# Optimization experiments

Hardware: AMD Instinct MI355X
Metric: run time of the kernel (lower is better)

Reference implementation:

```python
import jax, jax.numpy as jnp
import numpy as np

B, S, D = 2, 2048, 1024
H, DH = 16, 64          # n_heads, d_head = d_model // n_heads
WINDOW = 128            # sliding-window size (causal, includes self)


def setup_inputs() -> dict:
    key = jax.random.key(0)
    k1, k2, k3 = jax.random.split(key, 3)
    x = jax.random.normal(k1, (B, S, D), dtype=jnp.float32)
    w_qkv = jax.random.normal(k2, (D, 3 * D), dtype=jnp.float32) * (1.0 / np.sqrt(D))
    w_out = jax.random.normal(k3, (D, D), dtype=jnp.float32) * (1.0 / np.sqrt(D))
    return {"x": x, "w_qkv": w_qkv, "w_out": w_out}


def reference(x, w_qkv, w_out):
    b, s, d = x.shape
    # QKV projection (no bias): [B,S,3D] -> [B,S,3,H,DH]
    qkv = (x @ w_qkv).reshape(b, s, 3, H, DH)
    q, k, v = qkv[:, :, 0], qkv[:, :, 1], qkv[:, :, 2]  # each [B,S,H,DH]
    scale = 1.0 / np.sqrt(DH)
    # Dense scores [B,H,S,S], as the explicit-mask SDPA path computes
    scores = jnp.einsum("bihd,bjhd->bhij", q, k) * scale
    i = jnp.arange(s)[:, None]
    j = jnp.arange(s)[None, :]
    # allowed: causal AND within sliding window of WINDOW positions (incl. self)
    allowed = (j <= i) & (j > i - WINDOW)
    scores = jnp.where(allowed, scores, -jnp.inf)
    attn = jax.nn.softmax(scores, axis=-1)
    out = jnp.einsum("bhij,bjhd->bihd", attn, v).reshape(b, s, d)
    return out @ w_out
```

## Files before the change

kernel.cpp:

```cpp
#include <hip/hip_runtime.h>

#define SQ      2048
#define NB      2
#define NH      16
#define DHD     64
#define WIN     128
#define DMODEL  1024
#define TRIPLE  3072

typedef __attribute__((ext_vector_type(8))) short  short8;
typedef __attribute__((ext_vector_type(4))) float  f32x4;

__device__ __forceinline__ unsigned short f2bf(float f) {
  unsigned u = __float_as_uint(f);
  u += 0x7fff + ((u >> 16) & 1);
  return (unsigned short)(u >> 16);
}

__device__ __forceinline__ void load_lds16(const void* g, void* l) {
  __builtin_amdgcn_global_load_lds(
      (const __attribute__((address_space(1))) unsigned int*)g,
      (__attribute__((address_space(3))) unsigned int*)l, 16, 0, 0);
}

__global__ __launch_bounds__(256) void prep_kernel(
    const float* __restrict__ x, const float* __restrict__ w_qkv,
    const float* __restrict__ w_out,
    unsigned short* __restrict__ xb, unsigned short* __restrict__ wqkvT,
    unsigned short* __restrict__ woutT) {
  __shared__ float tile[32][33];
  int blk = blockIdx.x, tid = threadIdx.x;
  if (blk < 4096) {
    int idx = blk * 256 + tid;
    f32x4 v = ((const f32x4*)x)[idx];
    ushort4 o;
    o.x = f2bf(v[0]); o.y = f2bf(v[1]); o.z = f2bf(v[2]); o.w = f2bf(v[3]);
    ((ushort4*)xb)[idx] = o;
    return;
  }
  const float* in;
  unsigned short* out;
  int K = DMODEL, N, t;
  if (blk < 7168) { in = w_qkv; out = wqkvT; N = TRIPLE;  t = blk - 4096; }
  else            { in = w_out; out = woutT; N = DMODEL;  t = blk - 7168; }
  int ntiles = N / 32;
  int n0 = (t % ntiles) * 32, k0 = (t / ntiles) * 32;
  int tx = tid & 31, ty = tid >> 5;
#pragma unroll
  for (int r = 0; r < 4; ++r)
    tile[ty + 8 * r][tx] = in[(size_t)(k0 + ty + 8 * r) * N + (n0 + tx)];
  __syncthreads();
#pragma unroll
  for (int r = 0; r < 4; ++r)
    out[(size_t)(n0 + ty + 8 * r) * K + (k0 + tx)] = f2bf(tile[tx][ty + 8 * r]);
}

template <bool BF16OUT>
__global__ __launch_bounds__(512) void gemm_bt_kernel(
    const unsigned short* __restrict__ A,
    const unsigned short* __restrict__ Bt,
    void* __restrict__ Cv,
    int M, int N, int K) {
  __shared__ short lsA[128 * 64];
  __shared__ short lsB[128 * 64];
  int tid  = threadIdx.x;
  int wave = tid >> 6, lane = tid & 63;
  int quad = lane >> 4, l16 = lane & 15;
  int wm = (wave & 3) * 32;
  int wn = (wave >> 2) * 64;
  int m0 = blockIdx.x * 128, n0 = blockIdx.y * 128;

  f32x4 acc[2][4] = {};

  const short* Ag = (const short*)A;
  const short* Bg = (const short*)Bt;

  int row8 = lane >> 3;
  int gcol = ((lane & 7) ^ row8) * 8;
  int sw = (l16 & 7) * 8;

  for (int k0 = 0; k0 < K; k0 += 64) {
    const short* Ab = Ag + (size_t)(m0 + wave * 16) * K + k0;
    const short* Bb = Bg + (size_t)(n0 + wave * 16) * K + k0;
#pragma unroll
    for (int inst = 0; inst < 2; ++inst) {
      int r = inst * 8 + row8;
      load_lds16(Ab + (size_t)r * K + gcol, &lsA[(wave * 16 + inst * 8) * 64]);
      load_lds16(Bb + (size_t)r * K + gcol, &lsB[(wave * 16 + inst * 8) * 64]);
    }
    __syncthreads();
#pragma unroll
    for (int ks = 0; ks < 2; ++ks) {
      int coff = ((ks * 32 + quad * 8) ^ sw);
      short8 af[2], bf[4];
#pragma unroll
      for (int t = 0; t < 2; ++t)
        af[t] = *(const short8*)(&lsA[(wm + t * 16 + l16) * 64 + coff]);
#pragma unroll
      for (int t = 0; t < 4; ++t)
        bf[t] = *(const short8*)(&lsB[(wn + t * 16 + l16) * 64 + coff]);
#pragma unroll
      for (int mt = 0; mt < 2; ++mt)
#pragma unroll
        for (int nt = 0; nt < 4; ++nt)
          acc[mt][nt] = __builtin_amdgcn_mfma_f32_16x16x32_bf16(
              af[mt], bf[nt], acc[mt][nt], 0, 0, 0);
    }
    __syncthreads();
  }
#pragma unroll
  for (int mt = 0; mt < 2; ++mt)
#pragma unroll
    for (int nt = 0; nt < 4; ++nt)
#pragma unroll
      for (int r = 0; r < 4; ++r) {
        int row = m0 + wm + mt * 16 + quad * 4 + r;
        int col = n0 + wn + nt * 16 + l16;
        if (BF16OUT)
          ((unsigned short*)Cv)[(size_t)row * N + col] = f2bf(acc[mt][nt][r]);
        else
          ((float*)Cv)[(size_t)row * N + col] = acc[mt][nt][r];
      }
}

#define KSTR 72
#define VSTR 200
#define PSTR 72
__global__ __launch_bounds__(256) void attn_kernel(
    const unsigned short* __restrict__ qkvb,
    unsigned short* __restrict__ attnout) {
  __shared__ short Kl[192 * KSTR];
  __shared__ short Vt[64 * VSTR];
  __shared__ short Pl[4][16 * PSTR];

  int i0 = blockIdx.x * 64, h = blockIdx.y, b = blockIdx.z;
  int tid = threadIdx.x, wave = tid >> 6, lane = tid & 63;
  int quad = lane >> 4, l16 = lane & 15;
  const unsigned short* base = qkvb + (size_t)b * SQ * TRIPLE;

  short8 qa[2];
  {
    int qi = i0 + wave * 16 + l16;
    const unsigned short* qrow = base + (size_t)qi * TRIPLE + h * DHD;
    qa[0] = *(const short8*)(qrow + quad * 8);
    qa[1] = *(const short8*)(qrow + 32 + quad * 8);
  }

  int jbase = (i0 >= WIN) ? (i0 - WIN) : 0;
  int nch = (i0 + 64 - jbase) >> 6;

  int srow_ = tid >> 3;
  int scol_ = (tid & 7) * 8;
  for (int p = 0; p < 2 * nch; ++p) {
    int r = p * 32 + srow_;
    int j = jbase + r;
    const unsigned short* kr = base + (size_t)j * TRIPLE + DMODEL + h * DHD + scol_;
    *(short8*)(&Kl[r * KSTR + scol_]) = *(const short8*)kr;
    const unsigned short* vr = base + (size_t)j * TRIPLE + 2 * DMODEL + h * DHD + scol_;
    short8 vv = *(const short8*)vr;
#pragma unroll
    for (int e = 0; e < 8; ++e)
      Vt[(scol_ + e) * VSTR + r] = vv[e];
  }
  __syncthreads();

  f32x4 o[4] = {};
  float mrow[4] = {-1e30f, -1e30f, -1e30f, -1e30f};
  float lrow[4] = {0.f, 0.f, 0.f, 0.f};
  int irow = i0 + wave * 16 + quad * 4;

  for (int c = 0; c < nch; ++c) {
    int jc = jbase + c * 64;

    f32x4 s[4] = {};
#pragma unroll
    for (int ks = 0; ks < 2; ++ks)
#pragma unroll
      for (int nt = 0; nt < 4; ++nt) {
        short8 bk = *(const short8*)(&Kl[(c * 64 + nt * 16 + l16) * KSTR + ks * 32 + quad * 8]);
        s[nt] = __builtin_amdgcn_mfma_f32_16x16x32_bf16(qa[ks], bk, s[nt], 0, 0, 0);
      }
#pragma unroll
    for (int nt = 0; nt < 4; ++nt)
#pragma unroll
      for (int r = 0; r < 4; ++r) {
        int i_ = irow + r;
        int j_ = jc + nt * 16 + l16;
        bool ok = (j_ <= i_) && (j_ > i_ - WIN);
        s[nt][r] = ok ? s[nt][r] * 0.125f : -1e30f;
      }
    float rm[4];
#pragma unroll
    for (int r = 0; r < 4; ++r)
      rm[r] = fmaxf(fmaxf(s[0][r], s[1][r]), fmaxf(s[2][r], s[3][r]));
#pragma unroll
    for (int off = 1; off < 16; off <<= 1)
#pragma unroll
      for (int r = 0; r < 4; ++r) rm[r] = fmaxf(rm[r], __shfl_xor(rm[r], off, 64));
    float al[4];
#pragma unroll
    for (int r = 0; r < 4; ++r) {
      float mn = fmaxf(mrow[r], rm[r]);
      al[r] = __expf(mrow[r] - mn);
      mrow[r] = mn;
    }
    f32x4 p[4];
#pragma unroll
    for (int nt = 0; nt < 4; ++nt)
#pragma unroll
      for (int r = 0; r < 4; ++r) p[nt][r] = __expf(s[nt][r] - mrow[r]);
    float rs[4];
#pragma unroll
    for (int r = 0; r < 4; ++r)
      rs[r] = (p[0][r] + p[1][r]) + (p[2][r] + p[3][r]);
#pragma unroll
    for (int off = 1; off < 16; off <<= 1)
#pragma unroll
      for (int r = 0; r < 4; ++r) rs[r] += __shfl_xor(rs[r], off, 64);
#pragma unroll
    for (int r = 0; r < 4; ++r) lrow[r] = lrow[r] * al[r] + rs[r];
#pragma unroll
    for (int nt = 0; nt < 4; ++nt)
#pragma unroll
      for (int r = 0; r < 4; ++r) o[nt][r] *= al[r];
#pragma unroll
    for (int nt = 0; nt < 4; ++nt)
#pragma unroll
      for (int r = 0; r < 4; ++r)
        Pl[wave][(quad * 4 + r) * PSTR + nt * 16 + l16] = f2bf(p[nt][r]);
    short8 pa[2];
    pa[0] = *(const short8*)(&Pl[wave][l16 * PSTR + quad * 8]);
    pa[1] = *(const short8*)(&Pl[wave][l16 * PSTR + 32 + quad * 8]);
#pragma unroll
    for (int ks = 0; ks < 2; ++ks)
#pragma unroll
      for (int nt = 0; nt < 4; ++nt) {
        short8 bv = *(const short8*)(&Vt[(nt * 16 + l16) * VSTR + c * 64 + ks * 32 + quad * 8]);
        o[nt] = __builtin_amdgcn_mfma_f32_16x16x32_bf16(pa[ks], bv, o[nt], 0, 0, 0);
      }
  }

  float inv[4];
#pragma unroll
  for (int r = 0; r < 4; ++r) inv[r] = 1.0f / lrow[r];
#pragma unroll
  for (int nt = 0; nt < 4; ++nt)
#pragma unroll
    for (int r = 0; r < 4; ++r) {
      int i_ = irow + r;
      int d_ = nt * 16 + l16;
      attnout[(size_t)(b * SQ + i_) * DMODEL + h * DHD + d_] = f2bf(o[nt][r] * inv[r]);
    }
}

extern "C" void kernel_launch(void* const* d_in, const int* in_sizes, int n_in,
                              void* d_out, int out_size, void* d_ws, size_t ws_size,
                              hipStream_t stream) {
  const float* x     = (const float*)d_in[0];
  const float* w_qkv = (const float*)d_in[1];
  const float* w_out = (const float*)d_in[2];
  float* out = (float*)d_out;

  char* ws = (char*)d_ws;
  unsigned short* xb    = (unsigned short*)(ws);
  unsigned short* wqkvT = (unsigned short*)(ws + 8388608);
  unsigned short* woutT = (unsigned short*)(ws + 14680064);
  unsigned short* qkvb  = (unsigned short*)(ws + 16777216);
  unsigned short* attn  = (unsigned short*)(ws + 41943040);

  prep_kernel<<<8192, 256, 0, stream>>>(x, w_qkv, w_out, xb, wqkvT, woutT);
  gemm_bt_kernel<true><<<dim3((NB * SQ) / 128, TRIPLE / 128), 512, 0, stream>>>(
      xb, wqkvT, qkvb, NB * SQ, TRIPLE, DMODEL);
  attn_kernel<<<dim3(SQ / 64, NH, NB), 256, 0, stream>>>(qkvb, attn);
  gemm_bt_kernel<false><<<dim3((NB * SQ) / 128, DMODEL / 128), 512, 0, stream>>>(
      attn, woutT, out, NB * SQ, DMODEL, DMODEL);
}
```

Measured before the change: 150.8 us.

## Replace QKV projection GEMM with 256x256-tile eight-phase pipelined kernel

Adds a new bf16 MFMA GEMM with 256x256 output tiles per 512-thread block. It double-buffers LDS through direct global-to-LDS loads interleaved across four compute phases, uses XOR-swizzled LDS addressing, raises wave priority during MFMA, and remaps workgroups with a swizzle. Only the QKV projection uses it, which is meant to hide load latency and raise data reuse per tile. The trade-offs are larger LDS use (128KB), many more accumulator registers, and fewer blocks (192) to spread across the GPU.

```diff
diff --git a/kernel.cpp b/kernel.cpp
--- a/kernel.cpp
+++ b/kernel.cpp
@@ -123,6 +123,169 @@
       }
 }
 
+template <int M, int N, int K, bool BF16OUT>
+__global__ __launch_bounds__(512) void gemm8p_kernel(
+    const unsigned short* __restrict__ A,
+    const unsigned short* __restrict__ Bt,
+    void* __restrict__ Cv) {
+  constexpr int NT  = K / 64;
+  constexpr int NBN = N / 256;
+  __shared__ short lsA[2][256 * 64];
+  __shared__ short lsB[2][256 * 64];
+
+  const int tid  = threadIdx.x;
+  const int wave = tid >> 6, lane = tid & 63;
+  const int quad = lane >> 4, l16 = lane & 15;
+  const int wm = (wave >> 2) * 128;
+  const int wn = (wave & 3) * 64;
+
+  const int nwg = gridDim.x;
+  const int swz = ((int)blockIdx.x & 7) * (nwg >> 3) + ((int)blockIdx.x >> 3);
+  const int m0 = (swz / NBN) * 256, n0 = (swz % NBN) * 256;
+
+  const short* Ag = (const short*)A + (size_t)m0 * K;
+  const short* Bg = (const short*)Bt + (size_t)n0 * K;
+
+  const int r8 = lane >> 3;
+  const int gc = ((lane & 7) ^ r8) * 8;
+  const int sw = (l16 & 7) * 8;
+  const int wrow = wave * 16;
+
+  f32x4 acc[8][4] = {};
+  short8 bf[4];
+
+#define SBAR0() __builtin_amdgcn_sched_barrier(0)
+#define PHASE_BAR()                                   \
+  do { SBAR0(); __builtin_amdgcn_s_barrier(); SBAR0(); } while (0)
+#define STAGE_HALF(lds, g)                                                        \
+  do {                                                                            \
+    load_lds16((g) + (size_t)(wrow + r8) * K + gc, (lds) + wrow * 64);            \
+    load_lds16((g) + (size_t)(wrow + 8 + r8) * K + gc, (lds) + (wrow + 8) * 64);  \
+  } while (0)
+#define ST_A(t, h) STAGE_HALF(&lsA[(t) & 1][(h) * (128 * 64)],                    \
+                              Ag + (size_t)((h) * 128) * K + (t) * 64)
+#define ST_B(t, h) STAGE_HALF(&lsB[(t) & 1][(h) * (128 * 64)],                    \
+                              Bg + (size_t)((h) * 128) * K + (t) * 64)
+
+  ST_A(0, 0); ST_A(0, 1); ST_B(0, 0); ST_B(0, 1);
+  ST_A(1, 0); ST_A(1, 1); ST_B(1, 0); ST_B(1, 1);
+  asm volatile("s_waitcnt vmcnt(8)" ::: "memory");
+  PHASE_BAR();
+
+  for (int t = 0; t < NT; ++t) {
+    short* la = lsA[t & 1];
+    short* lb = lsB[t & 1];
+    const bool pre1 = (t > 0) && (t + 1 < NT);
+
+    {
+      const int coff = (quad * 8) ^ sw;
+      short8 af[4];
+#pragma unroll
+      for (int i = 0; i < 4; ++i)
+        af[i] = *(const short8*)(&la[(wm + i * 16 + l16) * 64 + coff]);
+#pragma unroll
+      for (int n = 0; n < 4; ++n)
+        bf[n] = *(const short8*)(&lb[(wn + n * 16 + l16) * 64 + coff]);
+      if (pre1) ST_A(t + 1, 0);
+      PHASE_BAR();
+      asm volatile("s_waitcnt lgkmcnt(0)" ::: "memory");
+      SBAR0();
+      __builtin_amdgcn_s_setprio(1);
+#pragma unroll
+      for (int i = 0; i < 4; ++i)
+#pragma unroll
+        for (int n = 0; n < 4; ++n)
+          acc[i][n] = __builtin_amdgcn_mfma_f32_16x16x32_bf16(af[i], bf[n], acc[i][n], 0, 0, 0);
+      __builtin_amdgcn_s_setprio(0);
+      PHASE_BAR();
+    }
+    {
+      const int coff = (quad * 8) ^ sw;
+      short8 af[4];
+#pragma unroll
+      for (int i = 0; i < 4; ++i)
+        af[i] = *(const short8*)(&la[(wm + 64 + i * 16 + l16) * 64 + coff]);
+      if (pre1) ST_A(t + 1, 1);
+      PHASE_BAR();
+      asm volatile("s_waitcnt lgkmcnt(0)" ::: "memory");
+      SBAR0();
+      __builtin_amdgcn_s_setprio(1);
+#pragma unroll
+      for (int i = 0; i < 4; ++i)
+#pragma unroll
+        for (int n = 0; n < 4; ++n)
+          acc[4 + i][n] = __builtin_amdgcn_mfma_f32_16x16x32_bf16(af[i], bf[n], acc[4 + i][n], 0, 0, 0);
+      __builtin_amdgcn_s_setprio(0);
+      PHASE_BAR();
+    }
+    {
+      const int coff = (32 + quad * 8) ^ sw;
+      short8 af[4];
+#pragma unroll
+      for (int i = 0; i < 4; ++i)
+        af[i] = *(const short8*)(&la[(wm + i * 16 + l16) * 64 + coff]);
+#pragma unroll
+      for (int n = 0; n < 4; ++n)
+        bf[n] = *(const short8*)(&lb[(wn + n * 16 + l16) * 64 + coff]);
+      if (pre1) ST_B(t + 1, 1);
+      PHASE_BAR();
+      asm volatile("s_waitcnt lgkmcnt(0)" ::: "memory");
+      SBAR0();
+      __builtin_amdgcn_s_setprio(1);
+#pragma unroll
+      for (int i = 0; i < 4; ++i)
+#pragma unroll
+        for (int n = 0; n < 4; ++n)
+          acc[i][n] = __builtin_amdgcn_mfma_f32_16x16x32_bf16(af[i], bf[n], acc[i][n], 0, 0, 0);
+      __builtin_amdgcn_s_setprio(0);
+      PHASE_BAR();
+    }
+    {
+      const int coff = (32 + quad * 8) ^ sw;
+      short8 af[4];
+#pragma unroll
+      for (int i = 0; i < 4; ++i)
+        af[i] = *(const short8*)(&la[(wm + 64 + i * 16 + l16) * 64 + coff]);
+      if (t + 2 < NT) ST_B(t + 2, 0);
+      PHASE_BAR();
+      asm volatile("s_waitcnt lgkmcnt(0)" ::: "memory");
+      SBAR0();
+      __builtin_amdgcn_s_setprio(1);
+#pragma unroll
+      for (int i = 0; i < 4; ++i)
+#pragma unroll
+        for (int n = 0; n < 4; ++n)
+          acc[4 + i][n] = __builtin_amdgcn_mfma_f32_16x16x32_bf16(af[i], bf[n], acc[4 + i][n], 0, 0, 0);
+      __builtin_amdgcn_s_setprio(0);
+      if (t + 2 < NT) {
+        asm volatile("s_waitcnt vmcnt(2)" ::: "memory");
+      } else if (t + 1 < NT) {
+        asm volatile("s_waitcnt vmcnt(0)" ::: "memory");
+      }
+      PHASE_BAR();
+    }
+  }
+#undef ST_B
+#undef ST_A
+#undef STAGE_HALF
+#undef PHASE_BAR
+#undef SBAR0
+
+#pragma unroll
+  for (int m = 0; m < 8; ++m)
+#pragma unroll
+    for (int n = 0; n < 4; ++n)
+#pragma unroll
+      for (int r = 0; r < 4; ++r) {
+        int row = m0 + wm + m * 16 + quad * 4 + r;
+        int col = n0 + wn + n * 16 + l16;
+        if (BF16OUT)
+          ((unsigned short*)Cv)[(size_t)row * N + col] = f2bf(acc[m][n][r]);
+        else
+          ((float*)Cv)[(size_t)row * N + col] = acc[m][n][r];
+      }
+}
+
 #define KSTR 72
 #define VSTR 200
 #define PSTR 72
@@ -269,8 +432,8 @@
   unsigned short* attn  = (unsigned short*)(ws + 41943040);
 
   prep_kernel<<<8192, 256, 0, stream>>>(x, w_qkv, w_out, xb, wqkvT, woutT);
-  gemm_bt_kernel<true><<<dim3((NB * SQ) / 128, TRIPLE / 128), 512, 0, stream>>>(
-      xb, wqkvT, qkvb, NB * SQ, TRIPLE, DMODEL);
+  gemm8p_kernel<NB * SQ, TRIPLE, DMODEL, true>
+      <<<(NB * SQ / 256) * (TRIPLE / 256), 512, 0, stream>>>(xb, wqkvT, qkvb);
   attn_kernel<<<dim3(SQ / 64, NH, NB), 256, 0, stream>>>(qkvb, attn);
   gemm_bt_kernel<false><<<dim3((NB * SQ) / 128, DMODEL / 128), 512, 0, stream>>>(
       attn, woutT, out, NB * SQ, DMODEL, DMODEL);
```

New measurement: 161.1 us. +6.9%, slower.
